# Kernel optimization log

Hardware: AMD Instinct MI355X
Metric: run time of the kernel (lower is better)

The kernel has to match this reference:

```python
import jax, jax.numpy as jnp
import numpy as np

B, IN, H = 256, 256, 512


def setup_inputs() -> dict:
    key = jax.random.key(0)
    ks = jax.random.split(key, 16)
    s = 0.02  # weight init scale
    d = {
        "x": jax.random.normal(ks[0], (B, IN), jnp.float32),
        "C_prev": jax.random.normal(ks[1], (B, H, H), jnp.float32) * 0.1,
        "n_prev": jax.random.normal(ks[2], (B, H), jnp.float32) * 0.1,
    }
    for j, nm in enumerate(["q", "k", "v", "i", "f", "o"]):
        d["W" + nm] = jax.random.normal(ks[3 + 2 * j], (H, IN), jnp.float32) * s
        d["b" + nm] = jnp.zeros((H,), jnp.float32)
    return d


def reference(x, C_prev, n_prev, Wq, bq, Wk, bk, Wv, bv, Wi, bi, Wf, bf, Wo, bo):
    # x: [B, In]; C_prev: [B, H, H]; n_prev: [B, H]
    h = Wq.shape[0]
    inv_sqrt_h = 1.0 / jnp.sqrt(jnp.asarray(h, x.dtype))
    q = x @ Wq.T + bq                              # [B, H]
    k = (x @ Wk.T + bk) * inv_sqrt_h               # [B, H] (scaled key)
    v = x @ Wv.T + bv                              # [B, H]
    i = jnp.exp(x @ Wi.T + bi)                     # exponential input gate
    f = jax.nn.sigmoid(x @ Wf.T + bf)              # forget gate
    o = jax.nn.sigmoid(x @ Wo.T + bo)              # output gate
    # Gates broadcast over the LAST axis of the [H, H] matrix state,
    # matching f * C_prev / i * jnp.outer(v, k) in the original.
    C_t = f[:, None, :] * C_prev + i[:, None, :] * (v[:, :, None] * k[:, None, :])  # [B, H, H]
    n_t = f * n_prev + i * k                       # [B, H]
    denom = jnp.maximum(jnp.abs(jnp.einsum("bh,bh->b", n_t, q)), 1.0)  # [B]
    h_t = o * (jnp.einsum("bij,bj->bi", C_t, q) / denom[:, None])      # [B, H]
    return (C_t, n_t, h_t)
```

## Files before the change

### kernel.cpp

```cpp
#include <hip/hip_runtime.h>
#include <math.h>

#define BATCH 256
#define INDIM 256
#define HDIM  512
#define BH    (BATCH * HDIM)

typedef float f32x4 __attribute__((ext_vector_type(4)));

__device__ __forceinline__ float sigmoidf_(float v) {
    return 1.0f / (1.0f + expf(-v));
}

__global__ __launch_bounds__(256) void gates_kernel(
    const float* __restrict__ x,
    const float* __restrict__ Wq, const float* __restrict__ bq,
    const float* __restrict__ Wk, const float* __restrict__ bk,
    const float* __restrict__ Wv, const float* __restrict__ bv,
    const float* __restrict__ Wi, const float* __restrict__ bi,
    const float* __restrict__ Wf, const float* __restrict__ bf,
    const float* __restrict__ Wo, const float* __restrict__ bo,
    float* __restrict__ gates)
{
    __shared__ float Wt[64][65];
    __shared__ float Xt[64][65];

    const int m0 = blockIdx.x * 64;
    const int n0 = blockIdx.y * 64;
    const int t  = threadIdx.x;

    const int g  = m0 >> 9;
    const int h0 = m0 & 511;

    const float* W; const float* bias;
    switch (g) {
        case 0: W = Wq; bias = bq; break;
        case 1: W = Wk; bias = bk; break;
        case 2: W = Wv; bias = bv; break;
        case 3: W = Wi; bias = bi; break;
        case 4: W = Wf; bias = bf; break;
        default: W = Wo; bias = bo; break;
    }
    const float* Wg = W + (size_t)h0 * INDIM;

    const int tx = t & 15;
    const int ty = t >> 4;

    float acc[4][4] = {};

    for (int k0 = 0; k0 < INDIM; k0 += 64) {
        const int kk4 = (t & 15) * 4;
        const int row = t >> 4;
        #pragma unroll
        for (int rr = 0; rr < 4; rr++) {
            const int mr = row + rr * 16;
            const float4 w = *(const float4*)(Wg + mr * INDIM + k0 + kk4);
            Wt[mr][kk4 + 0] = w.x; Wt[mr][kk4 + 1] = w.y;
            Wt[mr][kk4 + 2] = w.z; Wt[mr][kk4 + 3] = w.w;
            const float4 xv = *(const float4*)(x + (n0 + mr) * INDIM + k0 + kk4);
            Xt[mr][kk4 + 0] = xv.x; Xt[mr][kk4 + 1] = xv.y;
            Xt[mr][kk4 + 2] = xv.z; Xt[mr][kk4 + 3] = xv.w;
        }
        __syncthreads();
        #pragma unroll 8
        for (int kk = 0; kk < 64; kk++) {
            float a[4], bb[4];
            #pragma unroll
            for (int i2 = 0; i2 < 4; i2++) a[i2] = Xt[ty * 4 + i2][kk];
            #pragma unroll
            for (int j = 0; j < 4; j++) bb[j] = Wt[tx * 4 + j][kk];
            #pragma unroll
            for (int i2 = 0; i2 < 4; i2++)
                #pragma unroll
                for (int j = 0; j < 4; j++)
                    acc[i2][j] += a[i2] * bb[j];
        }
        __syncthreads();
    }

    const float inv_sqrt_h = 0.044194173824159216f;
    const int hb = h0 + tx * 4;
    const float4 b4 = *(const float4*)(bias + hb);

    #pragma unroll
    for (int i2 = 0; i2 < 4; i2++) {
        const int n = n0 + ty * 4 + i2;
        float4 r;
        r.x = acc[i2][0] + b4.x;
        r.y = acc[i2][1] + b4.y;
        r.z = acc[i2][2] + b4.z;
        r.w = acc[i2][3] + b4.w;
        if (g == 1) {
            r.x *= inv_sqrt_h; r.y *= inv_sqrt_h;
            r.z *= inv_sqrt_h; r.w *= inv_sqrt_h;
        } else if (g == 3) {
            r.x = expf(r.x); r.y = expf(r.y);
            r.z = expf(r.z); r.w = expf(r.w);
        } else if (g >= 4) {
            r.x = sigmoidf_(r.x); r.y = sigmoidf_(r.y);
            r.z = sigmoidf_(r.z); r.w = sigmoidf_(r.w);
        }
        *(float4*)(gates + (size_t)g * BH + (size_t)n * HDIM + hb) = r;
    }
}

__global__ __launch_bounds__(256) void cell_kernel(
    const float* __restrict__ C_prev,
    const float* __restrict__ gates,
    const float* __restrict__ n_prev,
    float* __restrict__ n_out,
    float* __restrict__ C_out,
    float* __restrict__ h_out)
{
    const int blk    = blockIdx.x;
    const int b      = blk >> 4;
    const int rchunk = blk & 15;
    const int t      = threadIdx.x;
    const int wave   = t >> 6;
    const int lane   = t & 63;

    const float* qb = gates + 0 * (size_t)BH + (size_t)b * HDIM;
    const float* kb = gates + 1 * (size_t)BH + (size_t)b * HDIM;
    const float* vb = gates + 2 * (size_t)BH + (size_t)b * HDIM;
    const float* ib = gates + 3 * (size_t)BH + (size_t)b * HDIM;
    const float* fb = gates + 4 * (size_t)BH + (size_t)b * HDIM;
    const float* ob = gates + 5 * (size_t)BH + (size_t)b * HDIM;
    const float* npv = n_prev + (size_t)b * HDIM;

    const int c0 = lane * 4;

    const float4 f0 = *(const float4*)(fb + c0);
    const float4 f1 = *(const float4*)(fb + 256 + c0);
    const float4 q0 = *(const float4*)(qb + c0);
    const float4 q1 = *(const float4*)(qb + 256 + c0);
    const float4 i0 = *(const float4*)(ib + c0);
    const float4 i1 = *(const float4*)(ib + 256 + c0);
    const float4 k0 = *(const float4*)(kb + c0);
    const float4 k1 = *(const float4*)(kb + 256 + c0);

    const float nt0 = fb[t] * npv[t] + ib[t] * kb[t];
    const float nt1 = fb[t + 256] * npv[t + 256] + ib[t + 256] * kb[t + 256];
    if (rchunk == 0) {
        n_out[(size_t)b * HDIM + t]       = nt0;
        n_out[(size_t)b * HDIM + t + 256] = nt1;
    }
    float p = nt0 * qb[t] + nt1 * qb[t + 256];
    #pragma unroll
    for (int off = 32; off > 0; off >>= 1)
        p += __shfl_down(p, off);

    __shared__ float red[4];
    __shared__ float dsh;
    if (lane == 0) red[wave] = p;
    __syncthreads();
    if (t == 0)
        dsh = 1.0f / fmaxf(fabsf(red[0] + red[1] + red[2] + red[3]), 1.0f);
    __syncthreads();
    const float dinv = dsh;

    float4 a0, a1;
    a0.x = i0.x * k0.x; a0.y = i0.y * k0.y; a0.z = i0.z * k0.z; a0.w = i0.w * k0.w;
    a1.x = i1.x * k1.x; a1.y = i1.y * k1.y; a1.z = i1.z * k1.z; a1.w = i1.w * k1.w;

    const size_t base = (size_t)b * HDIM * HDIM;
    const int r0 = rchunk * 32 + wave * 8;

    #pragma unroll
    for (int grp = 0; grp < 2; grp++) {
        const int rb = r0 + grp * 4;

        f32x4 cA[4], cB[4];
        #pragma unroll
        for (int rr = 0; rr < 4; rr++) {
            const float* cp = C_prev + base + (size_t)(rb + rr) * HDIM;
            cA[rr] = __builtin_nontemporal_load((const f32x4*)(cp + c0));
            cB[rr] = __builtin_nontemporal_load((const f32x4*)(cp + 256 + c0));
        }

        float dots[4];
        #pragma unroll
        for (int rr = 0; rr < 4; rr++) {
            const int r = rb + rr;
            const float vr = vb[r];

            f32x4 t0, t1;
            t0.x = f0.x * cA[rr].x + vr * a0.x;
            t0.y = f0.y * cA[rr].y + vr * a0.y;
            t0.z = f0.z * cA[rr].z + vr * a0.z;
            t0.w = f0.w * cA[rr].w + vr * a0.w;
            t1.x = f1.x * cB[rr].x + vr * a1.x;
            t1.y = f1.y * cB[rr].y + vr * a1.y;
            t1.z = f1.z * cB[rr].z + vr * a1.z;
            t1.w = f1.w * cB[rr].w + vr * a1.w;

            float* co = C_out + base + (size_t)r * HDIM;
            __builtin_nontemporal_store(t0, (f32x4*)(co + c0));
            __builtin_nontemporal_store(t1, (f32x4*)(co + 256 + c0));

            dots[rr] = t0.x * q0.x + t0.y * q0.y + t0.z * q0.z + t0.w * q0.w
                     + t1.x * q1.x + t1.y * q1.y + t1.z * q1.z + t1.w * q1.w;
        }

        #pragma unroll
        for (int rr = 0; rr < 4; rr++) {
            float d = dots[rr];
            #pragma unroll
            for (int off = 32; off > 0; off >>= 1)
                d += __shfl_down(d, off);
            if (lane == 0)
                h_out[(size_t)b * HDIM + rb + rr] = ob[rb + rr] * d * dinv;
        }
    }
}

extern "C" void kernel_launch(void* const* d_in, const int* in_sizes, int n_in,
                              void* d_out, int out_size, void* d_ws, size_t ws_size,
                              hipStream_t stream) {
    const float* x      = (const float*)d_in[0];
    const float* C_prev = (const float*)d_in[1];
    const float* n_prev = (const float*)d_in[2];
    const float* Wq = (const float*)d_in[3];  const float* bq = (const float*)d_in[4];
    const float* Wk = (const float*)d_in[5];  const float* bk = (const float*)d_in[6];
    const float* Wv = (const float*)d_in[7];  const float* bv = (const float*)d_in[8];
    const float* Wi = (const float*)d_in[9];  const float* bi = (const float*)d_in[10];
    const float* Wf = (const float*)d_in[11]; const float* bf = (const float*)d_in[12];
    const float* Wo = (const float*)d_in[13]; const float* bo = (const float*)d_in[14];

    float* out   = (float*)d_out;
    float* C_out = out;
    float* n_out = out + (size_t)BATCH * HDIM * HDIM;
    float* h_out = n_out + (size_t)BATCH * HDIM;

    float* gates = (float*)d_ws;

    dim3 gridA(3072 / 64, BATCH / 64);
    gates_kernel<<<gridA, 256, 0, stream>>>(x, Wq, bq, Wk, bk, Wv, bv,
                                            Wi, bi, Wf, bf, Wo, bo, gates);
    cell_kernel<<<BATCH * (HDIM / 32), 256, 0, stream>>>(C_prev, gates, n_prev,
                                                         n_out, C_out, h_out);
}
```

Baseline: 474.4 us.

## Vectorize gates GEMM LDS reads with swizzle and coarsen cell kernel rows per block

The gates GEMM now stores and reads shared-memory tiles as float4, using an XOR swizzle on the weight tile to avoid bank conflicts, which cuts the LDS instruction count. The cell kernel uses 4 blocks per batch row instead of 16, with each wave handling 32 rows, so the per-block gate loads and the n_t/denominator reduction are repeated far fewer times. The denominator is now computed per wave with a butterfly xor-shuffle, removing two __syncthreads. In exchange there are fewer blocks (1024) and a longer serial loop per wave, which may reduce memory-level parallelism in this bandwidth-bound kernel.

```diff
diff --git a/kernel.cpp b/kernel.cpp
--- a/kernel.cpp
+++ b/kernel.cpp
@@ -22,8 +22,8 @@
     const float* __restrict__ Wo, const float* __restrict__ bo,
     float* __restrict__ gates)
 {
-    __shared__ float Wt[64][65];
-    __shared__ float Xt[64][65];
+    __shared__ float Wt[64][68];
+    __shared__ float Xt[64][68];
 
     const int m0 = blockIdx.x * 64;
     const int n0 = blockIdx.y * 64;
@@ -45,6 +45,7 @@
 
     const int tx = t & 15;
     const int ty = t >> 4;
+    const int xsw = (tx & 7) << 2;
 
     float acc[4][4] = {};
 
@@ -55,25 +56,27 @@
         for (int rr = 0; rr < 4; rr++) {
             const int mr = row + rr * 16;
             const float4 w = *(const float4*)(Wg + mr * INDIM + k0 + kk4);
-            Wt[mr][kk4 + 0] = w.x; Wt[mr][kk4 + 1] = w.y;
-            Wt[mr][kk4 + 2] = w.z; Wt[mr][kk4 + 3] = w.w;
+            const int wc = kk4 ^ (((mr >> 2) & 7) << 2);
+            *(float4*)&Wt[mr][wc] = w;
             const float4 xv = *(const float4*)(x + (n0 + mr) * INDIM + k0 + kk4);
-            Xt[mr][kk4 + 0] = xv.x; Xt[mr][kk4 + 1] = xv.y;
-            Xt[mr][kk4 + 2] = xv.z; Xt[mr][kk4 + 3] = xv.w;
+            *(float4*)&Xt[mr][kk4] = xv;
         }
         __syncthreads();
-        #pragma unroll 8
-        for (int kk = 0; kk < 64; kk++) {
-            float a[4], bb[4];
-            #pragma unroll
-            for (int i2 = 0; i2 < 4; i2++) a[i2] = Xt[ty * 4 + i2][kk];
-            #pragma unroll
-            for (int j = 0; j < 4; j++) bb[j] = Wt[tx * 4 + j][kk];
+        #pragma unroll
+        for (int kk = 0; kk < 64; kk += 4) {
+            float4 ax[4], bw[4];
+            #pragma unroll
+            for (int i2 = 0; i2 < 4; i2++)
+                ax[i2] = *(const float4*)&Xt[ty * 4 + i2][kk];
+            #pragma unroll
+            for (int j = 0; j < 4; j++)
+                bw[j] = *(const float4*)&Wt[tx * 4 + j][kk ^ xsw];
             #pragma unroll
             for (int i2 = 0; i2 < 4; i2++)
                 #pragma unroll
                 for (int j = 0; j < 4; j++)
-                    acc[i2][j] += a[i2] * bb[j];
+                    acc[i2][j] += ax[i2].x * bw[j].x + ax[i2].y * bw[j].y
+                                + ax[i2].z * bw[j].z + ax[i2].w * bw[j].w;
         }
         __syncthreads();
     }
@@ -104,7 +107,7 @@
     }
 }
 
-__global__ __launch_bounds__(256) void cell_kernel(
+__global__ __launch_bounds__(256, 4) void cell_kernel(
     const float* __restrict__ C_prev,
     const float* __restrict__ gates,
     const float* __restrict__ n_prev,
@@ -113,8 +116,8 @@
     float* __restrict__ h_out)
 {
     const int blk    = blockIdx.x;
-    const int b      = blk >> 4;
-    const int rchunk = blk & 15;
+    const int b      = blk >> 2;
+    const int rchunk = blk & 3;
     const int t      = threadIdx.x;
     const int wave   = t >> 6;
     const int lane   = t & 63;
@@ -138,35 +141,32 @@
     const float4 k0 = *(const float4*)(kb + c0);
     const float4 k1 = *(const float4*)(kb + 256 + c0);
 
-    const float nt0 = fb[t] * npv[t] + ib[t] * kb[t];
-    const float nt1 = fb[t + 256] * npv[t + 256] + ib[t + 256] * kb[t + 256];
-    if (rchunk == 0) {
-        n_out[(size_t)b * HDIM + t]       = nt0;
-        n_out[(size_t)b * HDIM + t + 256] = nt1;
-    }
-    float p = nt0 * qb[t] + nt1 * qb[t + 256];
-    #pragma unroll
-    for (int off = 32; off > 0; off >>= 1)
-        p += __shfl_down(p, off);
-
-    __shared__ float red[4];
-    __shared__ float dsh;
-    if (lane == 0) red[wave] = p;
-    __syncthreads();
-    if (t == 0)
-        dsh = 1.0f / fmaxf(fabsf(red[0] + red[1] + red[2] + red[3]), 1.0f);
-    __syncthreads();
-    const float dinv = dsh;
-
     float4 a0, a1;
     a0.x = i0.x * k0.x; a0.y = i0.y * k0.y; a0.z = i0.z * k0.z; a0.w = i0.w * k0.w;
     a1.x = i1.x * k1.x; a1.y = i1.y * k1.y; a1.z = i1.z * k1.z; a1.w = i1.w * k1.w;
 
+    const float4 np0 = *(const float4*)(npv + c0);
+    const float4 np1 = *(const float4*)(npv + 256 + c0);
+    float4 nt0, nt1;
+    nt0.x = f0.x * np0.x + a0.x;  nt0.y = f0.y * np0.y + a0.y;
+    nt0.z = f0.z * np0.z + a0.z;  nt0.w = f0.w * np0.w + a0.w;
+    nt1.x = f1.x * np1.x + a1.x;  nt1.y = f1.y * np1.y + a1.y;
+    nt1.z = f1.z * np1.z + a1.z;  nt1.w = f1.w * np1.w + a1.w;
+    if (rchunk == 0 && wave == 0) {
+        *(float4*)(n_out + (size_t)b * HDIM + c0)       = nt0;
+        *(float4*)(n_out + (size_t)b * HDIM + 256 + c0) = nt1;
+    }
+    float p = nt0.x * q0.x + nt0.y * q0.y + nt0.z * q0.z + nt0.w * q0.w
+            + nt1.x * q1.x + nt1.y * q1.y + nt1.z * q1.z + nt1.w * q1.w;
+    #pragma unroll
+    for (int off = 32; off > 0; off >>= 1)
+        p += __shfl_xor(p, off);
+    const float dinv = 1.0f / fmaxf(fabsf(p), 1.0f);
+
     const size_t base = (size_t)b * HDIM * HDIM;
-    const int r0 = rchunk * 32 + wave * 8;
-
-    #pragma unroll
-    for (int grp = 0; grp < 2; grp++) {
+    const int r0 = rchunk * 128 + wave * 32;
+
+    for (int grp = 0; grp < 8; ++grp) {
         const int rb = r0 + grp * 4;
 
         f32x4 cA[4], cB[4];
@@ -176,12 +176,16 @@
             cA[rr] = __builtin_nontemporal_load((const f32x4*)(cp + c0));
             cB[rr] = __builtin_nontemporal_load((const f32x4*)(cp + 256 + c0));
         }
+        const float4 v4 = *(const float4*)(vb + rb);
+        const float4 o4 = *(const float4*)(ob + rb);
+        const float vr4[4] = {v4.x, v4.y, v4.z, v4.w};
+        const float or4[4] = {o4.x, o4.y, o4.z, o4.w};
 
         float dots[4];
         #pragma unroll
         for (int rr = 0; rr < 4; rr++) {
             const int r = rb + rr;
-            const float vr = vb[r];
+            const float vr = vr4[rr];
 
             f32x4 t0, t1;
             t0.x = f0.x * cA[rr].x + vr * a0.x;
@@ -208,7 +212,7 @@
             for (int off = 32; off > 0; off >>= 1)
                 d += __shfl_down(d, off);
             if (lane == 0)
-                h_out[(size_t)b * HDIM + rb + rr] = ob[rb + rr] * d * dinv;
+                h_out[(size_t)b * HDIM + rb + rr] = or4[rr] * d * dinv;
         }
     }
 }
@@ -236,6 +240,6 @@
     dim3 gridA(3072 / 64, BATCH / 64);
     gates_kernel<<<gridA, 256, 0, stream>>>(x, Wq, bq, Wk, bk, Wv, bv,
                                             Wi, bi, Wf, bf, Wo, bo, gates);
-    cell_kernel<<<BATCH * (HDIM / 32), 256, 0, stream>>>(C_prev, gates, n_prev,
-                                                         n_out, C_out, h_out);
-}
+    cell_kernel<<<BATCH * 4, 256, 0, stream>>>(C_prev, gates, n_prev,
+                                               n_out, C_out, h_out);
+}
```

Measured after the change: 491.5 us. +3.6%, slower.
